# Performance work log

Hardware: AMD Instinct MI355X
Metric: run time of the kernel (lower is better)

Reference implementation:

```python
import jax, jax.numpy as jnp
import numpy as np

BLOCK = 16          # NVFP4 block size along contraction dim
FP4_MAX = 6.0       # max magnitude of E2M1
FP8_MAX = 448.0     # max magnitude of float8_e4m3fn

_LEVELS = jnp.array([0.0, 0.5, 1.0, 1.5, 2.0, 3.0, 4.0, 6.0], dtype=jnp.float32)
_MIDS   = jnp.array([0.25, 0.75, 1.25, 1.75, 2.5, 3.5, 5.0], dtype=jnp.float32)


def quantize_dequant_nvfp4(t, global_scale):
    """Fake-quantize t (last dim % 16 == 0) to NVFP4: per-16-block fp8-e4m3
    scale times global fp32 scale, values snapped to the E2M1 grid."""
    shp = t.shape
    tb = t.reshape(shp[:-1] + (shp[-1] // BLOCK, BLOCK))
    amax = jnp.max(jnp.abs(tb), axis=-1, keepdims=True)
    # per-block scale, quantized to float8_e4m3fn as in TensorCoreNVFP4Layout
    bs = amax / (FP4_MAX * global_scale)
    bs8 = bs.astype(jnp.float8_e4m3fn).astype(jnp.float32)
    scale = bs8 * global_scale                       # effective dequant scale
    v = tb / jnp.maximum(scale, 1e-12)
    sign = jnp.sign(v)
    a = jnp.clip(jnp.abs(v), 0.0, FP4_MAX)
    idx = jnp.sum(a[..., None] > _MIDS, axis=-1)     # nearest E2M1 level
    q = _LEVELS[idx] * sign * scale
    return q.reshape(shp)


def setup_inputs() -> dict:
    key = jax.random.key(0)
    kx, kw, kb = jax.random.split(key, 3)
    x = jax.random.normal(kx, (8192, 4096), dtype=jnp.float32)
    weight = jax.random.normal(kw, (4096, 4096), dtype=jnp.float32) * 0.02
    bias = jax.random.normal(kb, (4096,), dtype=jnp.float32) * 0.02
    # global scales (weight_scale_2 / input_scale): amax / (6 * 448)
    input_scale = jnp.max(jnp.abs(x)) / (FP4_MAX * FP8_MAX)
    weight_scale = jnp.max(jnp.abs(weight)) / (FP4_MAX * FP8_MAX)
    return {"x": x, "weight": weight, "bias": bias,
            "input_scale": input_scale, "weight_scale": weight_scale}


def reference(x, weight, bias, input_scale, weight_scale):
    xq = quantize_dequant_nvfp4(x, input_scale)      # [T, K]
    wq = quantize_dequant_nvfp4(weight, weight_scale)  # [N, K]
    return jnp.einsum('tk,nk->tn', xq, wq) + bias    # F.linear
```

## Files before the change

### kernel.cpp

```cpp
#include <hip/hip_runtime.h>
#include <hip/hip_bf16.h>
#include <stdint.h>

typedef __attribute__((ext_vector_type(8))) __bf16 bf16x8;
typedef __attribute__((ext_vector_type(4))) float f32x4;
typedef __attribute__((ext_vector_type(4))) unsigned int u32x4;

#define BM 256
#define BN 256
#define BKT 32
#define SLOT 16384


__device__ __forceinline__ float fp8_e4m3_rne(float x) {
  if (x < 0.015625f) {
    return rintf(x * 512.0f) * 0.001953125f;
  }
  uint32_t u = __float_as_uint(x);
  uint32_t keep = u & 0xFFF00000u;
  uint32_t rem  = u & 0x000FFFFFu;
  uint32_t lsb  = (u >> 20) & 1u;
  if (rem > 0x80000u || (rem == 0x80000u && lsb)) keep += 0x100000u;
  return __uint_as_float(keep);
}

__device__ __forceinline__ float snap_lvl(float a) {
  if (a > 5.0f)  return 6.0f;
  if (a > 3.5f)  return 4.0f;
  if (a > 2.5f)  return 3.0f;
  if (a > 1.75f) return 2.0f;
  if (a > 1.25f) return 1.5f;
  if (a > 0.75f) return 1.0f;
  if (a > 0.25f) return 0.5f;
  return 0.0f;
}

__global__ __launch_bounds__(256) void quant_nvfp4(
    const float* __restrict__ in, unsigned short* __restrict__ out,
    const float* __restrict__ gsp, int nblk) {
  int b = blockIdx.x * 256 + threadIdx.x;
  if (b >= nblk) return;
  float gs = gsp[0];
  const float4* p = reinterpret_cast<const float4*>(in) + (size_t)b * 4;
  float v[16];
#pragma unroll
  for (int i = 0; i < 4; ++i) {
    float4 t4 = p[i];
    v[i * 4 + 0] = t4.x; v[i * 4 + 1] = t4.y;
    v[i * 4 + 2] = t4.z; v[i * 4 + 3] = t4.w;
  }
  float amax = 0.0f;
#pragma unroll
  for (int i = 0; i < 16; ++i) amax = fmaxf(amax, fabsf(v[i]));
  float bs8 = fp8_e4m3_rne(amax / (6.0f * gs));
  float scale = fmaxf(bs8 * gs, 1e-12f);
  unsigned short o[16];
#pragma unroll
  for (int i = 0; i < 16; ++i) {
    float q = v[i] / scale;
    float a = fminf(fabsf(q), 6.0f);
    float val = copysignf(snap_lvl(a) * bs8, q);
    o[i] = (unsigned short)(__float_as_uint(val) >> 16);
  }
  uint4 w0 = make_uint4((uint32_t)o[0] | ((uint32_t)o[1] << 16),
                        (uint32_t)o[2] | ((uint32_t)o[3] << 16),
                        (uint32_t)o[4] | ((uint32_t)o[5] << 16),
                        (uint32_t)o[6] | ((uint32_t)o[7] << 16));
  uint4 w1 = make_uint4((uint32_t)o[8]  | ((uint32_t)o[9]  << 16),
                        (uint32_t)o[10] | ((uint32_t)o[11] << 16),
                        (uint32_t)o[12] | ((uint32_t)o[13] << 16),
                        (uint32_t)o[14] | ((uint32_t)o[15] << 16));
  uint4* op = reinterpret_cast<uint4*>(out + (size_t)b * 16);
  op[0] = w0;
  op[1] = w1;
}


__device__ __forceinline__ void async_lds16(const void* g, void* l) {
  __builtin_amdgcn_global_load_lds((__attribute__((address_space(1))) void*)(g),
                                   (__attribute__((address_space(3))) void*)(l),
                                   16, 0, 0);
}

#define DSR(dst, a) asm volatile("ds_read_b128 %0, %1" : "=v"(dst) : "v"(a))
#define LGKM(N) do { asm volatile("s_waitcnt lgkmcnt(" #N ")" ::: "memory"); \
                     __builtin_amdgcn_sched_barrier(0); } while (0)
#define BCB(x) __builtin_bit_cast(bf16x8, x)

#define MF4(mi, ar, b0, b1, b2, b3) do {                                       \
    acc[mi][0] = __builtin_amdgcn_mfma_f32_16x16x32_bf16(BCB(ar), BCB(b0), acc[mi][0], 0, 0, 0); \
    acc[mi][1] = __builtin_amdgcn_mfma_f32_16x16x32_bf16(BCB(ar), BCB(b1), acc[mi][1], 0, 0, 0); \
    acc[mi][2] = __builtin_amdgcn_mfma_f32_16x16x32_bf16(BCB(ar), BCB(b2), acc[mi][2], 0, 0, 0); \
    acc[mi][3] = __builtin_amdgcn_mfma_f32_16x16x32_bf16(BCB(ar), BCB(b3), acc[mi][3], 0, 0, 0); \
  } while (0)

#define STAGE(tile, soff) {                                                    \
    char* _la = (char*)As + (soff);                                            \
    char* _lb = (char*)Bs + (soff);                                            \
    async_lds16(pA0 + (size_t)(tile) * BKT, _la + lo0);                        \
    async_lds16(pB0 + (size_t)(tile) * BKT, _lb + lo0);                        \
    async_lds16(pA1 + (size_t)(tile) * BKT, _la + lo1);                        \
    async_lds16(pB1 + (size_t)(tile) * BKT, _lb + lo1);                        \
  }

#define WINDOW(VMSTR, ta, oa, ob, o3, o4, DO3, DO4) do {                       \
    u32x4 rb0, rb1, rb2, rb3, ra0, ra1, ra2, ra3, ra4, ra5, ra6, ra7;          \
    u32x4 qb0, qb1, qb2, qb3, qa0, qa1, qa2, qa3, qa4, qa5, qa6, qa7;          \
    asm volatile("s_waitcnt vmcnt(" VMSTR ")" ::: "memory");                   \
    __builtin_amdgcn_s_barrier();                                              \
    if (DO3) STAGE((ta) + 3, o3);                                              \
    if (DO4) STAGE((ta) + 4, o4);                                              \
    DSR(rb0, adB[0] + (oa)); DSR(rb1, adB[1] + (oa));                          \
    DSR(rb2, adB[2] + (oa)); DSR(rb3, adB[3] + (oa));                          \
    DSR(ra0, adA[0] + (oa)); DSR(ra1, adA[1] + (oa));                          \
    DSR(ra2, adA[2] + (oa)); DSR(ra3, adA[3] + (oa));                          \
    DSR(ra4, adA[4] + (oa)); DSR(ra5, adA[5] + (oa));                          \
    DSR(ra6, adA[6] + (oa)); DSR(ra7, adA[7] + (oa));                          \
    __builtin_amdgcn_sched_barrier(0);                                         \
    LGKM(7); __builtin_amdgcn_s_setprio(1); MF4(0, ra0, rb0, rb1, rb2, rb3);   \
    LGKM(6); MF4(1, ra1, rb0, rb1, rb2, rb3);                                  \
    LGKM(5); MF4(2, ra2, rb0, rb1, rb2, rb3);                                  \
    LGKM(4); MF4(3, ra3, rb0, rb1, rb2, rb3);                                  \
    LGKM(3); MF4(4, ra4, rb0, rb1, rb2, rb3);                                  \
    DSR(qb0, adB[0] + (ob)); DSR(qb1, adB[1] + (ob));                          \
    DSR(qb2, adB[2] + (ob)); DSR(qb3, adB[3] + (ob));                          \
    DSR(qa0, adA[0] + (ob)); DSR(qa1, adA[1] + (ob));                          \
    DSR(qa2, adA[2] + (ob)); DSR(qa3, adA[3] + (ob));                          \
    __builtin_amdgcn_sched_barrier(0);                                         \
    LGKM(10); MF4(5, ra5, rb0, rb1, rb2, rb3);                                 \
    LGKM(9);  MF4(6, ra6, rb0, rb1, rb2, rb3);                                 \
    LGKM(8);  MF4(7, ra7, rb0, rb1, rb2, rb3);                                 \
    DSR(qa4, adA[4] + (ob)); DSR(qa5, adA[5] + (ob));                          \
    DSR(qa6, adA[6] + (ob)); DSR(qa7, adA[7] + (ob));                          \
    __builtin_amdgcn_sched_barrier(0);                                         \
    LGKM(7); MF4(0, qa0, qb0, qb1, qb2, qb3);                                  \
    LGKM(6); MF4(1, qa1, qb0, qb1, qb2, qb3);                                  \
    LGKM(5); MF4(2, qa2, qb0, qb1, qb2, qb3);                                  \
    LGKM(4); MF4(3, qa3, qb0, qb1, qb2, qb3);                                  \
    LGKM(3); MF4(4, qa4, qb0, qb1, qb2, qb3);                                  \
    LGKM(2); MF4(5, qa5, qb0, qb1, qb2, qb3);                                  \
    LGKM(1); MF4(6, qa6, qb0, qb1, qb2, qb3);                                  \
    LGKM(0); MF4(7, qa7, qb0, qb1, qb2, qb3);                                  \
    __builtin_amdgcn_s_setprio(0);                                             \
    __builtin_amdgcn_sched_barrier(0);                                         \
  } while (0)

__global__ __launch_bounds__(512, 2) void gemm_bt_bf16(
    const unsigned short* __restrict__ A, const unsigned short* __restrict__ B,
    const float* __restrict__ bias, const float* __restrict__ gsx,
    const float* __restrict__ gsw, float* __restrict__ C,
    int M, int N, int K) {
  __shared__ __align__(16) unsigned short As[5 * 8192];
  __shared__ __align__(16) unsigned short Bs[5 * 8192];

  const int t = threadIdx.x;
  const int l = t & 63;
  const int w = t >> 6;
  const int wm = w >> 2, wn = w & 3;

  const int nbn = N / BN;
  const int nwg = (M / BM) * nbn;
  const int cpx = nwg >> 3;
  int bid = blockIdx.x;
  int logical = (bid & 7) * cpx + (bid >> 3);
  const int bm = logical / nbn, bn = logical % nbn;
  const int brow = bm * BM, bcol = bn * BN;

  unsigned int b0 = (unsigned int)t * 16u;
  unsigned int b1 = b0 + 8192u;
  unsigned int bp0 = b0 ^ (((b0 >> 7) & 3u) << 4);
  unsigned int bp1 = b1 ^ (((b1 >> 7) & 3u) << 4);
  const unsigned int lo0 = b0, lo1 = b1;
  const unsigned short* pA0 = A + (size_t)(brow + (bp0 >> 6)) * K + ((bp0 & 63u) >> 1);
  const unsigned short* pA1 = A + (size_t)(brow + (bp1 >> 6)) * K + ((bp1 & 63u) >> 1);
  const unsigned short* pB0 = B + (size_t)(bcol + (bp0 >> 6)) * K + ((bp0 & 63u) >> 1);
  const unsigned short* pB1 = B + (size_t)(bcol + (bp1 >> 6)) * K + ((bp1 & 63u) >> 1);

  const unsigned baseAu = (unsigned)(uintptr_t)(&As[0]);
  const unsigned baseBu = (unsigned)(uintptr_t)(&Bs[0]);
  unsigned int adA[8], adB[4];
#pragma unroll
  for (int mi = 0; mi < 8; ++mi) {
    unsigned int r = wm * 128 + mi * 16 + (l & 15);
    unsigned int q = r * 64 + ((l >> 4) << 4);
    adA[mi] = baseAu + (q ^ (((q >> 7) & 3u) << 4));
  }
#pragma unroll
  for (int ni = 0; ni < 4; ++ni) {
    unsigned int r = wn * 64 + ni * 16 + (l & 15);
    unsigned int q = r * 64 + ((l >> 4) << 4);
    adB[ni] = baseBu + (q ^ (((q >> 7) & 3u) << 4));
  }

  f32x4 acc[8][4] = {};

  STAGE(0, 0);
  STAGE(1, SLOT);
  STAGE(2, 2 * SLOT);

  int sa = 0;
#pragma unroll 1
  for (int k = 0; k < 62; ++k) {
    int ta = 2 * k;
    int sb = sa + 1; if (sb >= 5) sb -= 5;
    int s3 = sa + 3; if (s3 >= 5) s3 -= 5;
    int s4 = sa + 4; if (s4 >= 5) s4 -= 5;
    WINDOW("4", ta, sa * SLOT, sb * SLOT, s3 * SLOT, s4 * SLOT, 1, 1);
    sa += 2; if (sa >= 5) sa -= 5;
  }
  WINDOW("4", 124, 4 * SLOT, 0 * SLOT, 2 * SLOT, 0, 1, 0);
  WINDOW("0", 126, 1 * SLOT, 2 * SLOT, 0, 0, 0, 0);

  const float gscale = gsx[0] * gsw[0];
  float bias_r[4];
#pragma unroll
  for (int ni = 0; ni < 4; ++ni)
    bias_r[ni] = bias[bcol + wn * 64 + ni * 16 + (l & 15)];
#pragma unroll
  for (int mi = 0; mi < 8; ++mi) {
#pragma unroll
    for (int ni = 0; ni < 4; ++ni) {
#pragma unroll
      for (int r = 0; r < 4; ++r) {
        int row = brow + wm * 128 + mi * 16 + (l >> 4) * 4 + r;
        int col = bcol + wn * 64 + ni * 16 + (l & 15);
        C[(size_t)row * N + col] = acc[mi][ni][r] * gscale + bias_r[ni];
      }
    }
  }
}


extern "C" void kernel_launch(void* const* d_in, const int* in_sizes, int n_in,
                              void* d_out, int out_size, void* d_ws, size_t ws_size,
                              hipStream_t stream) {
  const float* x    = (const float*)d_in[0];
  const float* wgt  = (const float*)d_in[1];
  const float* bias = (const float*)d_in[2];
  const float* isc  = (const float*)d_in[3];
  const float* wsc  = (const float*)d_in[4];
  float* out = (float*)d_out;

  const int N = in_sizes[2];
  const int K = in_sizes[1] / N;
  const int M = in_sizes[0] / K;

  unsigned short* Aq = (unsigned short*)d_ws;
  unsigned short* Bq = Aq + (size_t)M * K;

  int nblkA = M * K / 16;
  quant_nvfp4<<<(nblkA + 255) / 256, 256, 0, stream>>>(x, Aq, isc, nblkA);
  int nblkB = N * K / 16;
  quant_nvfp4<<<(nblkB + 255) / 256, 256, 0, stream>>>(wgt, Bq, wsc, nblkB);

  dim3 grid((M / BM) * (N / BN));
  gemm_bt_bf16<<<grid, 512, 0, stream>>>(Aq, Bq, bias, isc, wsc, out, M, N, K);
}
```

Before: 282.1 us.

## Split each K-tile into half-tile phases with finer-grained staging and LDS reads

Restructures the GEMM main loop from two-tile windows into per-tile phases. Each phase waits and barriers twice, issues half the global->LDS copies per phase, and prefetches the next tile's B and A fragments into registers while computing the second half of the current tile. The A-tile row mapping in LDS is permuted so each half of the staged A corresponds to the rows computed in each phase. This aims to spread VMEM and LDS traffic more evenly and overlap fragment loads with MFMA work, at the cost of more barriers and more live registers.

```diff
diff --git a/kernel.cpp b/kernel.cpp
--- a/kernel.cpp
+++ b/kernel.cpp
@@ -85,6 +85,7 @@
 #define DSR(dst, a) asm volatile("ds_read_b128 %0, %1" : "=v"(dst) : "v"(a))
 #define LGKM(N) do { asm volatile("s_waitcnt lgkmcnt(" #N ")" ::: "memory"); \
                      __builtin_amdgcn_sched_barrier(0); } while (0)
+#define VMC(S) asm volatile("s_waitcnt vmcnt(" S ")" ::: "memory")
 #define BCB(x) __builtin_bit_cast(bf16x8, x)
 
 #define MF4(mi, ar, b0, b1, b2, b3) do {                                       \
@@ -94,53 +95,43 @@
     acc[mi][3] = __builtin_amdgcn_mfma_f32_16x16x32_bf16(BCB(ar), BCB(b3), acc[mi][3], 0, 0, 0); \
   } while (0)
 
-#define STAGE(tile, soff) {                                                    \
-    char* _la = (char*)As + (soff);                                            \
-    char* _lb = (char*)Bs + (soff);                                            \
-    async_lds16(pA0 + (size_t)(tile) * BKT, _la + lo0);                        \
-    async_lds16(pB0 + (size_t)(tile) * BKT, _lb + lo0);                        \
-    async_lds16(pA1 + (size_t)(tile) * BKT, _la + lo1);                        \
-    async_lds16(pB1 + (size_t)(tile) * BKT, _lb + lo1);                        \
-  }
-
-#define WINDOW(VMSTR, ta, oa, ob, o3, o4, DO3, DO4) do {                       \
-    u32x4 rb0, rb1, rb2, rb3, ra0, ra1, ra2, ra3, ra4, ra5, ra6, ra7;          \
-    u32x4 qb0, qb1, qb2, qb3, qa0, qa1, qa2, qa3, qa4, qa5, qa6, qa7;          \
-    asm volatile("s_waitcnt vmcnt(" VMSTR ")" ::: "memory");                   \
+#define STG_A1(tile, so) async_lds16(pA0 + (size_t)(tile) * BKT, (char*)As + (so) + lo0)
+#define STG_B1(tile, so) async_lds16(pB0 + (size_t)(tile) * BKT, (char*)Bs + (so) + lo0)
+#define STG_B2(tile, so) async_lds16(pB1 + (size_t)(tile) * BKT, (char*)Bs + (so) + lo1)
+#define STG_A2(tile, so) async_lds16(pA1 + (size_t)(tile) * BKT, (char*)As + (so) + lo1)
+
+#define TILE(VM1, VM2, DO_S, sCur, sNxt, sStg, stgT, RN,                       \
+             bX0, bX1, bX2, bX3, bY0, bY1, bY2, bY3) do {                      \
+    VMC(VM1);                                                                  \
     __builtin_amdgcn_s_barrier();                                              \
-    if (DO3) STAGE((ta) + 3, o3);                                              \
-    if (DO4) STAGE((ta) + 4, o4);                                              \
-    DSR(rb0, adB[0] + (oa)); DSR(rb1, adB[1] + (oa));                          \
-    DSR(rb2, adB[2] + (oa)); DSR(rb3, adB[3] + (oa));                          \
-    DSR(ra0, adA[0] + (oa)); DSR(ra1, adA[1] + (oa));                          \
-    DSR(ra2, adA[2] + (oa)); DSR(ra3, adA[3] + (oa));                          \
-    DSR(ra4, adA[4] + (oa)); DSR(ra5, adA[5] + (oa));                          \
-    DSR(ra6, adA[6] + (oa)); DSR(ra7, adA[7] + (oa));                          \
-    __builtin_amdgcn_sched_barrier(0);                                         \
-    LGKM(7); __builtin_amdgcn_s_setprio(1); MF4(0, ra0, rb0, rb1, rb2, rb3);   \
-    LGKM(6); MF4(1, ra1, rb0, rb1, rb2, rb3);                                  \
-    LGKM(5); MF4(2, ra2, rb0, rb1, rb2, rb3);                                  \
-    LGKM(4); MF4(3, ra3, rb0, rb1, rb2, rb3);                                  \
-    LGKM(3); MF4(4, ra4, rb0, rb1, rb2, rb3);                                  \
-    DSR(qb0, adB[0] + (ob)); DSR(qb1, adB[1] + (ob));                          \
-    DSR(qb2, adB[2] + (ob)); DSR(qb3, adB[3] + (ob));                          \
-    DSR(qa0, adA[0] + (ob)); DSR(qa1, adA[1] + (ob));                          \
-    DSR(qa2, adA[2] + (ob)); DSR(qa3, adA[3] + (ob));                          \
-    __builtin_amdgcn_sched_barrier(0);                                         \
-    LGKM(10); MF4(5, ra5, rb0, rb1, rb2, rb3);                                 \
-    LGKM(9);  MF4(6, ra6, rb0, rb1, rb2, rb3);                                 \
-    LGKM(8);  MF4(7, ra7, rb0, rb1, rb2, rb3);                                 \
-    DSR(qa4, adA[4] + (ob)); DSR(qa5, adA[5] + (ob));                          \
-    DSR(qa6, adA[6] + (ob)); DSR(qa7, adA[7] + (ob));                          \
-    __builtin_amdgcn_sched_barrier(0);                                         \
-    LGKM(7); MF4(0, qa0, qb0, qb1, qb2, qb3);                                  \
-    LGKM(6); MF4(1, qa1, qb0, qb1, qb2, qb3);                                  \
-    LGKM(5); MF4(2, qa2, qb0, qb1, qb2, qb3);                                  \
-    LGKM(4); MF4(3, qa3, qb0, qb1, qb2, qb3);                                  \
-    LGKM(3); MF4(4, qa4, qb0, qb1, qb2, qb3);                                  \
-    LGKM(2); MF4(5, qa5, qb0, qb1, qb2, qb3);                                  \
-    LGKM(1); MF4(6, qa6, qb0, qb1, qb2, qb3);                                  \
-    LGKM(0); MF4(7, qa7, qb0, qb1, qb2, qb3);                                  \
+    if (DO_S) { STG_A1(stgT, sStg); STG_B1(stgT, sStg); }                      \
+    DSR(nA0, adA[4] + (sCur)); DSR(nA1, adA[5] + (sCur));                      \
+    DSR(nA2, adA[6] + (sCur)); DSR(nA3, adA[7] + (sCur));                      \
+    __builtin_amdgcn_sched_barrier(0);                                         \
+    LGKM(4);                                                                   \
+    __builtin_amdgcn_s_setprio(1);                                             \
+    MF4(0, aC0, bX0, bX1, bX2, bX3);                                           \
+    MF4(1, aC1, bX0, bX1, bX2, bX3);                                           \
+    MF4(2, aC2, bX0, bX1, bX2, bX3);                                           \
+    MF4(3, aC3, bX0, bX1, bX2, bX3);                                           \
+    __builtin_amdgcn_s_setprio(0);                                             \
+    __builtin_amdgcn_sched_barrier(0);                                         \
+    VMC(VM2);                                                                  \
+    __builtin_amdgcn_s_barrier();                                              \
+    if (DO_S) { STG_B2(stgT, sStg); STG_A2(stgT, sStg); }                      \
+    if (RN) {                                                                  \
+      DSR(bY0, adB[0] + (sNxt)); DSR(bY1, adB[1] + (sNxt));                    \
+      DSR(bY2, adB[2] + (sNxt)); DSR(bY3, adB[3] + (sNxt));                    \
+      DSR(aC0, adA[0] + (sNxt)); DSR(aC1, adA[1] + (sNxt));                    \
+      DSR(aC2, adA[2] + (sNxt)); DSR(aC3, adA[3] + (sNxt));                    \
+    }                                                                          \
+    __builtin_amdgcn_sched_barrier(0);                                         \
+    if (RN) { LGKM(8); } else { LGKM(0); }                                     \
+    __builtin_amdgcn_s_setprio(1);                                             \
+    MF4(4, nA0, bX0, bX1, bX2, bX3);                                           \
+    MF4(5, nA1, bX0, bX1, bX2, bX3);                                           \
+    MF4(6, nA2, bX0, bX1, bX2, bX3);                                           \
+    MF4(7, nA3, bX0, bX1, bX2, bX3);                                           \
     __builtin_amdgcn_s_setprio(0);                                             \
     __builtin_amdgcn_sched_barrier(0);                                         \
   } while (0)
@@ -168,48 +159,70 @@
 
   unsigned int b0 = (unsigned int)t * 16u;
   unsigned int b1 = b0 + 8192u;
-  unsigned int bp0 = b0 ^ (((b0 >> 7) & 3u) << 4);
-  unsigned int bp1 = b1 ^ (((b1 >> 7) & 3u) << 4);
+  unsigned int sp0 = b0 ^ (((b0 >> 7) & 3u) << 4);
+  unsigned int sp1 = b1 ^ (((b1 >> 7) & 3u) << 4);
   const unsigned int lo0 = b0, lo1 = b1;
-  const unsigned short* pA0 = A + (size_t)(brow + (bp0 >> 6)) * K + ((bp0 & 63u) >> 1);
-  const unsigned short* pA1 = A + (size_t)(brow + (bp1 >> 6)) * K + ((bp1 & 63u) >> 1);
-  const unsigned short* pB0 = B + (size_t)(bcol + (bp0 >> 6)) * K + ((bp0 & 63u) >> 1);
-  const unsigned short* pB1 = B + (size_t)(bcol + (bp1 >> 6)) * K + ((bp1 & 63u) >> 1);
+  unsigned int rA0 = b0 >> 6, rA1 = b1 >> 6;
+  unsigned int gA0 = ((rA0 >> 6) & 1u) * 128u + (rA0 >> 7) * 64u + (rA0 & 63u);
+  unsigned int gA1 = ((rA1 >> 6) & 1u) * 128u + (rA1 >> 7) * 64u + (rA1 & 63u);
+  const unsigned short* pA0 = A + (size_t)(brow + gA0) * K + ((sp0 & 63u) >> 1);
+  const unsigned short* pA1 = A + (size_t)(brow + gA1) * K + ((sp1 & 63u) >> 1);
+  const unsigned short* pB0 = B + (size_t)(bcol + (b0 >> 6)) * K + ((sp0 & 63u) >> 1);
+  const unsigned short* pB1 = B + (size_t)(bcol + (b1 >> 6)) * K + ((sp1 & 63u) >> 1);
 
   const unsigned baseAu = (unsigned)(uintptr_t)(&As[0]);
   const unsigned baseBu = (unsigned)(uintptr_t)(&Bs[0]);
   unsigned int adA[8], adB[4];
 #pragma unroll
   for (int mi = 0; mi < 8; ++mi) {
-    unsigned int r = wm * 128 + mi * 16 + (l & 15);
-    unsigned int q = r * 64 + ((l >> 4) << 4);
+    unsigned int rp = (unsigned)(mi >> 2) * 128u + (unsigned)wm * 64u +
+                      (unsigned)(mi & 3) * 16u + (l & 15);
+    unsigned int q = rp * 64u + (((unsigned)l >> 4) << 4);
     adA[mi] = baseAu + (q ^ (((q >> 7) & 3u) << 4));
   }
 #pragma unroll
   for (int ni = 0; ni < 4; ++ni) {
-    unsigned int r = wn * 64 + ni * 16 + (l & 15);
-    unsigned int q = r * 64 + ((l >> 4) << 4);
+    unsigned int r = (unsigned)wn * 64u + (unsigned)ni * 16u + (l & 15);
+    unsigned int q = r * 64u + (((unsigned)l >> 4) << 4);
     adB[ni] = baseBu + (q ^ (((q >> 7) & 3u) << 4));
   }
 
   f32x4 acc[8][4] = {};
-
-  STAGE(0, 0);
-  STAGE(1, SLOT);
-  STAGE(2, 2 * SLOT);
+  u32x4 aC0, aC1, aC2, aC3;
+  u32x4 nA0, nA1, nA2, nA3;
+  u32x4 bP0, bP1, bP2, bP3;
+  u32x4 bQ0, bQ1, bQ2, bQ3;
+
+  STG_A1(0, 0);        STG_B1(0, 0);        STG_B2(0, 0);        STG_A2(0, 0);
+  STG_A1(1, SLOT);     STG_B1(1, SLOT);     STG_B2(1, SLOT);     STG_A2(1, SLOT);
+  STG_A1(2, 2 * SLOT); STG_B1(2, 2 * SLOT); STG_B2(2, 2 * SLOT); STG_A2(2, 2 * SLOT);
+  VMC("9");
+  __builtin_amdgcn_s_barrier();
+  DSR(bP0, adB[0]); DSR(bP1, adB[1]); DSR(bP2, adB[2]); DSR(bP3, adB[3]);
+  DSR(aC0, adA[0]); DSR(aC1, adA[1]); DSR(aC2, adA[2]); DSR(aC3, adA[3]);
+  __builtin_amdgcn_sched_barrier(0);
 
   int sa = 0;
 #pragma unroll 1
-  for (int k = 0; k < 62; ++k) {
-    int ta = 2 * k;
-    int sb = sa + 1; if (sb >= 5) sb -= 5;
-    int s3 = sa + 3; if (s3 >= 5) s3 -= 5;
-    int s4 = sa + 4; if (s4 >= 5) s4 -= 5;
-    WINDOW("4", ta, sa * SLOT, sb * SLOT, s3 * SLOT, s4 * SLOT, 1, 1);
-    sa += 2; if (sa >= 5) sa -= 5;
-  }
-  WINDOW("4", 124, 4 * SLOT, 0 * SLOT, 2 * SLOT, 0, 1, 0);
-  WINDOW("0", 126, 1 * SLOT, 2 * SLOT, 0, 0, 0, 0);
+  for (int T = 0; T < 124; T += 2) {
+    int sb = sa + SLOT; if (sb >= 5 * SLOT) sb -= 5 * SLOT;
+    int s2 = sb + SLOT; if (s2 >= 5 * SLOT) s2 -= 5 * SLOT;
+    int s3 = s2 + SLOT; if (s3 >= 5 * SLOT) s3 -= 5 * SLOT;
+    int s4 = s3 + SLOT; if (s4 >= 5 * SLOT) s4 -= 5 * SLOT;
+    TILE("8", "7", 1, sa, sb, s3, T + 3, 1,
+         bP0, bP1, bP2, bP3, bQ0, bQ1, bQ2, bQ3);
+    TILE("8", "7", 1, sb, s2, s4, T + 4, 1,
+         bQ0, bQ1, bQ2, bQ3, bP0, bP1, bP2, bP3);
+    sa = s2;
+  }
+  TILE("8", "7", 1, 4 * SLOT, 0 * SLOT, 2 * SLOT, 127, 1,
+       bP0, bP1, bP2, bP3, bQ0, bQ1, bQ2, bQ3);
+  TILE("8", "5", 0, 0 * SLOT, 1 * SLOT, 0, 0, 1,
+       bQ0, bQ1, bQ2, bQ3, bP0, bP1, bP2, bP3);
+  TILE("4", "1", 0, 1 * SLOT, 2 * SLOT, 0, 0, 1,
+       bP0, bP1, bP2, bP3, bQ0, bQ1, bQ2, bQ3);
+  TILE("0", "0", 0, 2 * SLOT, 0, 0, 0, 0,
+       bQ0, bQ1, bQ2, bQ3, bP0, bP1, bP2, bP3);
 
   const float gscale = gsx[0] * gsw[0];
   float bias_r[4];
```

After: 284.8 us. Within noise of the previous version (+0.9%).
